# Performance work log

Measured on AMD Instinct MI355X. Metric: run time of the kernel, lower is better.

Reference implementation:

```python
import jax, jax.numpy as jnp
import numpy as np

N = 1_000_000
F_IN = 16
HID = 32
E = 16_000_000


def setup_inputs() -> dict:
    key = jax.random.key(0)
    ks = jax.random.split(key, 20)
    s = 0.1
    inp = {
        "x": jax.random.normal(ks[0], (N, F_IN), dtype=jnp.float32),
        "edge_index": jax.random.randint(ks[1], (2, E), 0, N, dtype=jnp.int64),
        "edge_weight": jax.random.uniform(ks[2], (E,), dtype=jnp.float32),
        # ChebConv(K=1) weights for the 3 GRU gates (x-side and h-side)
        "Wxz": jax.random.normal(ks[3], (F_IN, HID), dtype=jnp.float32) * s,
        "bxz": jnp.zeros((HID,), jnp.float32),
        "Whz": jax.random.normal(ks[4], (HID, HID), dtype=jnp.float32) * s,
        "bhz": jnp.zeros((HID,), jnp.float32),
        "Wxr": jax.random.normal(ks[5], (F_IN, HID), dtype=jnp.float32) * s,
        "bxr": jnp.zeros((HID,), jnp.float32),
        "Whr": jax.random.normal(ks[6], (HID, HID), dtype=jnp.float32) * s,
        "bhr": jnp.zeros((HID,), jnp.float32),
        "Wxh": jax.random.normal(ks[7], (F_IN, HID), dtype=jnp.float32) * s,
        "bxh": jnp.zeros((HID,), jnp.float32),
        "Whh": jax.random.normal(ks[8], (HID, HID), dtype=jnp.float32) * s,
        "bhh": jnp.zeros((HID,), jnp.float32),
        # final Linear(32, 1)
        "Wlin": jax.random.normal(ks[9], (HID, 1), dtype=jnp.float32) * s,
        "blin": jnp.zeros((1,), jnp.float32),
    }
    return inp


def _gconv_gru(x, Wxz, bxz, Whz, bhz, Wxr, bxr, Whr, bhr, Wxh, bxh, Whh, bhh):
    # GConvGRU with ChebConv K=1: each conv is T0(L)x @ W + b == x @ W + b
    # (edge_index / edge_weight are mathematically unused when K=1).
    H = jnp.zeros((x.shape[0], Whz.shape[0]), dtype=x.dtype)  # initial hidden state
    Z = jax.nn.sigmoid(x @ Wxz + bxz + H @ Whz + bhz)          # update gate
    R = jax.nn.sigmoid(x @ Wxr + bxr + H @ Whr + bhr)          # reset gate
    H_tilde = jnp.tanh(x @ Wxh + bxh + (R * H) @ Whh + bhh)    # candidate
    return Z * H + (1.0 - Z) * H_tilde


def reference(x, edge_index, edge_weight, Wxz, bxz, Whz, bhz, Wxr, bxr, Whr, bhr,
              Wxh, bxh, Whh, bhh, Wlin, blin):
    H = _gconv_gru(x, Wxz, bxz, Whz, bhz, Wxr, bxr, Whr, bhr, Wxh, bxh, Whh, bhh)
    h = jax.nn.relu(H)
    return h @ Wlin + blin  # [N, 1]
```

## Files before the change

kernel.cpp:

```cpp
#include <hip/hip_runtime.h>


typedef float v2f __attribute__((ext_vector_type(2)));
typedef float v4f __attribute__((ext_vector_type(4)));

constexpr int F   = 16;
constexpr int HD  = 32;
constexpr int NPT = 4;

__global__ __launch_bounds__(256, 2) void gru_fused(
    const float* __restrict__ x,
    const float* __restrict__ Wxz, const float* __restrict__ bxz,
    const float* __restrict__ bhz,
    const float* __restrict__ Wxh, const float* __restrict__ bxh,
    const float* __restrict__ bhh,
    const float* __restrict__ Wlin, const float* __restrict__ blin,
    float* __restrict__ out, int n)
{
    __shared__ alignas(16) v2f  sW[F * HD];
    __shared__ alignas(16) v2f  sB[HD];
    __shared__ alignas(16) float sL[HD];

    const int tid = threadIdx.x;

    #pragma unroll
    for (int i = 0; i < 2; ++i) {
        const int idx = tid + i * 256;
        sW[idx] = (v2f){ Wxz[idx], 2.0f * Wxh[idx] };
    }
    if (tid < HD) {
        sB[tid] = (v2f){ bxz[tid] + bhz[tid], 2.0f * (bxh[tid] + bhh[tid]) };
        sL[tid] = Wlin[tid];
    }
    __syncthreads();

    const int t = blockIdx.x * 256 + tid;
    const int base = t * NPT;
    if (base >= n) return;

    v2f xp[2][F];
    {
        const float4* px = reinterpret_cast<const float4*>(x + (size_t)base * F);
        #pragma unroll
        for (int p = 0; p < 2; ++p) {
            float4 n0[4], n1[4];
            #pragma unroll
            for (int q = 0; q < 4; ++q) { n0[q] = px[8*p + q]; n1[q] = px[8*p + q + 4]; }
            #pragma unroll
            for (int q = 0; q < 4; ++q) {
                xp[p][4*q+0] = (v2f){n0[q].x, n1[q].x};
                xp[p][4*q+1] = (v2f){n0[q].y, n1[q].y};
                xp[p][4*q+2] = (v2f){n0[q].z, n1[q].z};
                xp[p][4*q+3] = (v2f){n0[q].w, n1[q].w};
            }
        }
    }

    const float b0 = blin[0];
    v2f res[2];
    res[0] = (v2f){b0, b0};
    res[1] = (v2f){b0, b0};

    #pragma unroll 2
    for (int jp = 0; jp < HD / 2; ++jp) {
        const v4f bb = *reinterpret_cast<const v4f*>(&sB[2 * jp]);
        v2f aZ[2][2], aH[2][2];
        #pragma unroll
        for (int p = 0; p < 2; ++p) {
            aZ[0][p] = (v2f){bb[0], bb[0]};  aH[0][p] = (v2f){bb[1], bb[1]};
            aZ[1][p] = (v2f){bb[2], bb[2]};  aH[1][p] = (v2f){bb[3], bb[3]};
        }
        #pragma unroll
        for (int k = 0; k < F; ++k) {
            const v4f w = *reinterpret_cast<const v4f*>(&sW[k * HD + 2 * jp]);
            const v2f wz0 = {w[0], w[0]}, wh0 = {w[1], w[1]};
            const v2f wz1 = {w[2], w[2]}, wh1 = {w[3], w[3]};
            #pragma unroll
            for (int p = 0; p < 2; ++p) {
                const v2f xk = xp[p][k];
                aZ[0][p] = __builtin_elementwise_fma(xk, wz0, aZ[0][p]);
                aH[0][p] = __builtin_elementwise_fma(xk, wh0, aH[0][p]);
                aZ[1][p] = __builtin_elementwise_fma(xk, wz1, aZ[1][p]);
                aH[1][p] = __builtin_elementwise_fma(xk, wh1, aH[1][p]);
            }
        }
        const v2f wl = *reinterpret_cast<const v2f*>(&sL[2 * jp]);
        #pragma unroll
        for (int jj = 0; jj < 2; ++jj) {
            #pragma unroll
            for (int p = 0; p < 2; ++p) {
                #pragma unroll
                for (int h = 0; h < 2; ++h) {
                    const float az = aZ[jj][p][h];
                    const float ah = aH[jj][p][h];
                    const float u = __expf(az);
                    const float v = __expf(fminf(ah, 87.f));
                    const float r = __builtin_amdgcn_rcpf((1.f + u) * (1.f + v));
                    const float num = fmaxf(v - 1.f, 0.f);
                    res[p][h] = fmaf(num * r, wl[jj], res[p][h]);
                }
            }
        }
    }

    float4 o = make_float4(res[0][0], res[0][1], res[1][0], res[1][1]);
    *reinterpret_cast<float4*>(out + base) = o;
}

extern "C" void kernel_launch(void* const* d_in, const int* in_sizes, int n_in,
                              void* d_out, int out_size, void* d_ws, size_t ws_size,
                              hipStream_t stream) {
    const float* x    = (const float*)d_in[0];
    const float* Wxz  = (const float*)d_in[3];
    const float* bxz  = (const float*)d_in[4];
    const float* bhz  = (const float*)d_in[6];
    const float* Wxh  = (const float*)d_in[11];
    const float* bxh  = (const float*)d_in[12];
    const float* bhh  = (const float*)d_in[14];
    const float* Wlin = (const float*)d_in[15];
    const float* blin = (const float*)d_in[16];
    float* out = (float*)d_out;

    const int n = in_sizes[0] / F;
    const int threads = n / NPT;
    const int blocks = (threads + 255) / 256;
    gru_fused<<<blocks, 256, 0, stream>>>(
        x, Wxz, bxz, bhz, Wxh, bxh, bhh, Wlin, blin, out, n);
}
```

Baseline: 264.1 us.

## Split hidden dimension across two thread teams and reduce through shared memory

```diff
diff --git a/kernel.cpp b/kernel.cpp
--- a/kernel.cpp
+++ b/kernel.cpp
@@ -17,94 +17,116 @@
     const float* __restrict__ Wlin, const float* __restrict__ blin,
     float* __restrict__ out, int n)
 {
-    __shared__ alignas(16) v2f  sW[F * HD];
-    __shared__ alignas(16) v2f  sB[HD];
-    __shared__ alignas(16) float sL[HD];
+    __shared__ __align__(16) v2f   sW[F * HD];
+    __shared__ __align__(16) v2f   sB[HD];
+    __shared__ __align__(16) float sL[HD];
+    __shared__ __align__(16) float4 sRes[128];
 
-    const int tid = threadIdx.x;
+    const int tid    = threadIdx.x;
+    const int team   = tid >> 7;
+    const int pr     = tid & 127;
+    const int base   = (blockIdx.x * 128 + pr) * NPT;
+    const bool active = base < n;
+
+    constexpr float L2E = 1.4426950408889634f;
+
+    float4 xr[16];
+    if (active) {
+        const float4* px = reinterpret_cast<const float4*>(x + (size_t)base * F);
+        #pragma unroll
+        for (int q = 0; q < 16; ++q) xr[q] = px[q];
+    }
 
     #pragma unroll
     for (int i = 0; i < 2; ++i) {
         const int idx = tid + i * 256;
-        sW[idx] = (v2f){ Wxz[idx], 2.0f * Wxh[idx] };
+        sW[idx] = (v2f){ Wxz[idx] * L2E, Wxh[idx] * (2.f * L2E) };
     }
     if (tid < HD) {
-        sB[tid] = (v2f){ bxz[tid] + bhz[tid], 2.0f * (bxh[tid] + bhh[tid]) };
+        sB[tid] = (v2f){ (bxz[tid] + bhz[tid]) * L2E,
+                         (bxh[tid] + bhh[tid]) * (2.f * L2E) };
         sL[tid] = Wlin[tid];
     }
     __syncthreads();
 
-    const int t = blockIdx.x * 256 + tid;
-    const int base = t * NPT;
-    if (base >= n) return;
+    v2f res[2];
+    res[0] = (v2f){0.f, 0.f};
+    res[1] = (v2f){0.f, 0.f};
 
-    v2f xp[2][F];
-    {
-        const float4* px = reinterpret_cast<const float4*>(x + (size_t)base * F);
+    if (active) {
+        v2f xp[2][F];
         #pragma unroll
         for (int p = 0; p < 2; ++p) {
-            float4 n0[4], n1[4];
-            #pragma unroll
-            for (int q = 0; q < 4; ++q) { n0[q] = px[8*p + q]; n1[q] = px[8*p + q + 4]; }
             #pragma unroll
             for (int q = 0; q < 4; ++q) {
-                xp[p][4*q+0] = (v2f){n0[q].x, n1[q].x};
-                xp[p][4*q+1] = (v2f){n0[q].y, n1[q].y};
-                xp[p][4*q+2] = (v2f){n0[q].z, n1[q].z};
-                xp[p][4*q+3] = (v2f){n0[q].w, n1[q].w};
+                const float4 n0 = xr[8*p + q];
+                const float4 n1 = xr[8*p + 4 + q];
+                xp[p][4*q+0] = (v2f){n0.x, n1.x};
+                xp[p][4*q+1] = (v2f){n0.y, n1.y};
+                xp[p][4*q+2] = (v2f){n0.z, n1.z};
+                xp[p][4*q+3] = (v2f){n0.w, n1.w};
             }
         }
-    }
 
-    const float b0 = blin[0];
-    v2f res[2];
-    res[0] = (v2f){b0, b0};
-    res[1] = (v2f){b0, b0};
-
-    #pragma unroll 2
-    for (int jp = 0; jp < HD / 2; ++jp) {
-        const v4f bb = *reinterpret_cast<const v4f*>(&sB[2 * jp]);
-        v2f aZ[2][2], aH[2][2];
+        const int jp0 = team * 8;
         #pragma unroll
-        for (int p = 0; p < 2; ++p) {
-            aZ[0][p] = (v2f){bb[0], bb[0]};  aH[0][p] = (v2f){bb[1], bb[1]};
-            aZ[1][p] = (v2f){bb[2], bb[2]};  aH[1][p] = (v2f){bb[3], bb[3]};
-        }
-        #pragma unroll
-        for (int k = 0; k < F; ++k) {
-            const v4f w = *reinterpret_cast<const v4f*>(&sW[k * HD + 2 * jp]);
-            const v2f wz0 = {w[0], w[0]}, wh0 = {w[1], w[1]};
-            const v2f wz1 = {w[2], w[2]}, wh1 = {w[3], w[3]};
+        for (int jj = 0; jj < 8; ++jj) {
+            const int jp = jp0 + jj;
+            const v4f bb = *reinterpret_cast<const v4f*>(&sB[2 * jp]);
+            v2f aZ[2][2], aH[2][2];
             #pragma unroll
             for (int p = 0; p < 2; ++p) {
-                const v2f xk = xp[p][k];
-                aZ[0][p] = __builtin_elementwise_fma(xk, wz0, aZ[0][p]);
-                aH[0][p] = __builtin_elementwise_fma(xk, wh0, aH[0][p]);
-                aZ[1][p] = __builtin_elementwise_fma(xk, wz1, aZ[1][p]);
-                aH[1][p] = __builtin_elementwise_fma(xk, wh1, aH[1][p]);
+                aZ[0][p] = (v2f){bb[0], bb[0]};  aH[0][p] = (v2f){bb[1], bb[1]};
+                aZ[1][p] = (v2f){bb[2], bb[2]};  aH[1][p] = (v2f){bb[3], bb[3]};
             }
-        }
-        const v2f wl = *reinterpret_cast<const v2f*>(&sL[2 * jp]);
-        #pragma unroll
-        for (int jj = 0; jj < 2; ++jj) {
             #pragma unroll
-            for (int p = 0; p < 2; ++p) {
+            for (int k = 0; k < F; ++k) {
+                const v4f w = *reinterpret_cast<const v4f*>(&sW[k * HD + 2 * jp]);
+                const v2f wz0 = {w[0], w[0]}, wh0 = {w[1], w[1]};
+                const v2f wz1 = {w[2], w[2]}, wh1 = {w[3], w[3]};
                 #pragma unroll
-                for (int h = 0; h < 2; ++h) {
-                    const float az = aZ[jj][p][h];
-                    const float ah = aH[jj][p][h];
-                    const float u = __expf(az);
-                    const float v = __expf(fminf(ah, 87.f));
-                    const float r = __builtin_amdgcn_rcpf((1.f + u) * (1.f + v));
-                    const float num = fmaxf(v - 1.f, 0.f);
-                    res[p][h] = fmaf(num * r, wl[jj], res[p][h]);
+                for (int p = 0; p < 2; ++p) {
+                    const v2f xk = xp[p][k];
+                    aZ[0][p] = __builtin_elementwise_fma(xk, wz0, aZ[0][p]);
+                    aH[0][p] = __builtin_elementwise_fma(xk, wh0, aH[0][p]);
+                    aZ[1][p] = __builtin_elementwise_fma(xk, wz1, aZ[1][p]);
+                    aH[1][p] = __builtin_elementwise_fma(xk, wh1, aH[1][p]);
+                }
+            }
+            const v2f wl = *reinterpret_cast<const v2f*>(&sL[2 * jp]);
+            #pragma unroll
+            for (int j2 = 0; j2 < 2; ++j2) {
+                #pragma unroll
+                for (int p = 0; p < 2; ++p) {
+                    #pragma unroll
+                    for (int h = 0; h < 2; ++h) {
+                        const float az = aZ[j2][p][h];
+                        const float ah = aH[j2][p][h];
+                        const float u = __builtin_amdgcn_exp2f(az);
+                        const float v = __builtin_amdgcn_exp2f(fminf(ah, 87.f));
+                        const float r = __builtin_amdgcn_rcpf((1.f + u) * (1.f + v));
+                        const float num = fmaxf(v - 1.f, 0.f);
+                        res[p][h] = fmaf(num * r, wl[j2], res[p][h]);
+                    }
                 }
             }
         }
     }
 
-    float4 o = make_float4(res[0][0], res[0][1], res[1][0], res[1][1]);
-    *reinterpret_cast<float4*>(out + base) = o;
+    if (team == 1) {
+        sRes[pr] = make_float4(res[0][0], res[0][1], res[1][0], res[1][1]);
+    }
+    __syncthreads();
+    if (team == 0 && active) {
+        const float4 o  = sRes[pr];
+        const float  b0 = blin[0];
+        float4 w;
+        w.x = res[0][0] + o.x + b0;
+        w.y = res[0][1] + o.y + b0;
+        w.z = res[1][0] + o.z + b0;
+        w.w = res[1][1] + o.w + b0;
+        *reinterpret_cast<float4*>(out + base) = w;
+    }
 }
 
 extern "C" void kernel_launch(void* const* d_in, const int* in_sizes, int n_in,
@@ -122,8 +144,8 @@
     float* out = (float*)d_out;
 
     const int n = in_sizes[0] / F;
-    const int threads = n / NPT;
-    const int blocks = (threads + 255) / 256;
+    const int pairs  = n / NPT;
+    const int blocks = (pairs + 127) / 128;
     gru_fused<<<blocks, 256, 0, stream>>>(
         x, Wxz, bxz, bhz, Wxh, bxh, bhh, Wlin, blin, out, n);
 }
```

Measured after the change: 267.3 us. Within noise of the previous version (+1.2%).
